# Performance work log

Hardware: AMD Instinct MI355X
Metric: run time of the kernel (lower is better)

## Reference

```python
import jax, jax.numpy as jnp
import numpy as np

SHAPE = 512
DEPTH = 9


def setup_inputs() -> dict:
    key = jax.random.key(0)
    # points with x,y in [0,1) so int(pt*SHAPE) lands in [0, SHAPE-1]
    data = jax.random.uniform(key, (8, 200000, 4), dtype=jnp.float32)
    return {"data": data}


def _group_one(pts, shape, depth):
    # pts: [N, F]. Faithful to the torch loop: scale x,y by `shape`, bin into
    # (x, y) cells, assign each nonzero point (in original point order) to the
    # first free depth slot of its cell, storing fractional coords.
    n, f = pts.shape
    scale = jnp.ones((f,), pts.dtype).at[0].set(shape).at[1].set(shape)
    scaled = pts * scale
    nonzero = jnp.any(pts != 0, axis=-1)  # all-zero points are skipped
    xi = scaled[:, 0].astype(jnp.int32)  # int() truncation == floor for [0,1)
    yi = scaled[:, 1].astype(jnp.int32)
    cell = xi * shape + yi  # [N]
    ncells = shape * shape
    # sentinel cell for zero points so they don't consume slots
    cell_k = jnp.where(nonzero, cell, ncells)
    # slot = number of earlier nonzero points in the same cell.
    # Stable sort by cell preserves point order within each cell; rank within
    # the sorted segment is (position - segment start).
    order = jnp.argsort(cell_k)  # stable
    sc = cell_k[order]
    ar = jnp.arange(n, dtype=jnp.int32)
    is_start = jnp.concatenate([jnp.ones((1,), bool), sc[1:] != sc[:-1]])
    seg_start = jax.lax.cummax(jnp.where(is_start, ar, 0))
    rank_sorted = ar - seg_start
    slot = jnp.zeros((n,), jnp.int32).at[order].set(rank_sorted)
    # fractional in-cell coordinates (pt[0]-x, pt[1]-y), other features kept
    frac = scaled.at[:, 0].add(-xi.astype(scaled.dtype)).at[:, 1].add(-yi.astype(scaled.dtype))
    valid = nonzero & (slot < depth)  # overflow points are dropped (warning in torch)
    dump = ncells * depth  # scratch row for invalid points
    flat_idx = jnp.where(valid, cell * depth + slot, dump)
    grid = jnp.zeros((ncells * depth + 1, f), scaled.dtype)
    grid = grid.at[flat_idx].set(jnp.where(valid[:, None], frac, jnp.zeros_like(frac)))
    return grid[:-1].reshape(shape, shape, depth * f)


def reference(data) -> jnp.ndarray:
    # data: [B, N, F] -> [B, SHAPE, SHAPE, DEPTH*F]
    return jax.vmap(lambda p: _group_one(p, SHAPE, DEPTH))(data)
```

## Files before the change

kernel.cpp:

```cpp
#include <hip/hip_runtime.h>
#include <stdint.h>

#define SHAPE    512
#define DEPTH    9
#define NCELLS   (SHAPE * SHAPE)
#define NB       8
#define RANGES   1024
#define CR       (NCELLS / RANGES)
#define CRSHIFT  8
#define CAP      512
#define CAPSHIFT 9
#define NCHUNK   64
#define SENT     0xFFFFFFFFu
#define EMIT     ((CR * DEPTH) / 256)

typedef float f32x4 __attribute__((ext_vector_type(4)));


__global__ void zero_heads(unsigned* __restrict__ h, int n) {
    int t = blockIdx.x * blockDim.x + threadIdx.x;
    if (t < n) h[t] = 0u;
}

__global__ __launch_bounds__(512) void bin_kernel(const float4* __restrict__ pts,
                                                  unsigned* __restrict__ headcnt,
                                                  unsigned* __restrict__ bktE,
                                                  int nPerB, int chSz) {
    __shared__ unsigned h[RANGES];
    int b = blockIdx.x & (NB - 1);
    int c = blockIdx.x >> 3;
    for (int r = threadIdx.x; r < RANGES; r += 512) h[r] = 0u;
    __syncthreads();

    int i0 = c * chSz;
    int i1 = i0 + chSz; if (i1 > nPerB) i1 = nPerB;
    const float4* pb = pts + (size_t)b * nPerB;

    for (int i = i0 + threadIdx.x; i < i1; i += 512) {
        float4 p = pb[i];
        if (p.x == 0.f && p.y == 0.f && p.z == 0.f && p.w == 0.f) continue;
        int xi = (int)(p.x * (float)SHAPE);
        int yi = (int)(p.y * (float)SHAPE);
        unsigned cell = (unsigned)(xi * SHAPE + yi);
        if (cell >= (unsigned)NCELLS) continue;
        atomicAdd(&h[cell >> CRSHIFT], 1u);
    }
    __syncthreads();

    for (int r = threadIdx.x; r < RANGES; r += 512) {
        unsigned n = h[r];
        unsigned bucket = (unsigned)(b * RANGES + r);
        unsigned base = n ? atomicAdd(&headcnt[bucket], n) : 0u;
        h[r] = (bucket << CAPSHIFT) + base;
    }
    __syncthreads();

    for (int i = i0 + threadIdx.x; i < i1; i += 512) {
        float4 p = pb[i];
        if (p.x == 0.f && p.y == 0.f && p.z == 0.f && p.w == 0.f) continue;
        int xi = (int)(p.x * (float)SHAPE);
        int yi = (int)(p.y * (float)SHAPE);
        unsigned cell = (unsigned)(xi * SHAPE + yi);
        if (cell >= (unsigned)NCELLS) continue;
        unsigned r = cell >> CRSHIFT;
        unsigned pos = atomicAdd(&h[r], 1u);
        unsigned bucket = (unsigned)(b * RANGES) + r;
        if (pos < ((bucket + 1u) << CAPSHIFT))
            bktE[pos] = ((unsigned)i << CRSHIFT) | (cell & (CR - 1));
    }
}

__global__ __launch_bounds__(256) void group_kernel(const unsigned* __restrict__ headcnt,
                                                    const unsigned* __restrict__ bktE,
                                                    const float4* __restrict__ pts,
                                                    float4* __restrict__ out,
                                                    int nPerB) {
    __shared__ unsigned slots[CR * DEPTH];
    int blk = blockIdx.x;
    int b = blk & (NB - 1);
    int r = blk >> 3;
    int gblk = b * RANGES + r;

    uint4* s4 = (uint4*)slots;
    for (int k = threadIdx.x; k < (CR * DEPTH) / 4; k += 256)
        s4[k] = make_uint4(SENT, SENT, SENT, SENT);
    __syncthreads();

    unsigned n = headcnt[gblk];
    if (n > CAP) n = CAP;
    size_t base = (size_t)gblk << CAPSHIFT;

    for (unsigned t = threadIdx.x; t < n; t += 256) {
        unsigned v = bktE[base + t];
        unsigned* s = &slots[(v & (CR - 1)) * DEPTH];
#pragma unroll
        for (int d = 0; d < DEPTH; ++d) {
            unsigned old = atomicMin(&s[d], v);
            if (old == SENT) break;
            v = (v > old) ? v : old;
        }
    }
    __syncthreads();

    const float4* pb = pts + (size_t)b * nPerB;
    float4* ob = out + ((size_t)b * NCELLS + ((size_t)r << CRSHIFT)) * DEPTH;

    unsigned key[EMIT];
#pragma unroll
    for (int k = 0; k < EMIT; ++k)
        key[k] = slots[threadIdx.x + k * 256];

    float4 pv[EMIT];
#pragma unroll
    for (int k = 0; k < EMIT; ++k)
        if (key[k] != SENT) pv[k] = pb[key[k] >> CRSHIFT];

#pragma unroll
    for (int k = 0; k < EMIT; ++k) {
        f32x4 rv = (f32x4){0.f, 0.f, 0.f, 0.f};
        if (key[k] != SENT) {
            float sx = pv[k].x * (float)SHAPE;
            float sy = pv[k].y * (float)SHAPE;
            rv.x = sx - truncf(sx);
            rv.y = sy - truncf(sy);
            rv.z = pv[k].z;
            rv.w = pv[k].w;
        }
        __builtin_nontemporal_store(rv, (f32x4*)&ob[threadIdx.x + k * 256]);
    }
}


__global__ void init_kernel(uint4* __restrict__ A, int nVec4) {
    int tid = blockIdx.x * blockDim.x + threadIdx.x;
    if (tid < nVec4) A[tid] = make_uint4(SENT, SENT, SENT, SENT);
}

__global__ void cascade_kernel(const float4* __restrict__ pts,
                               unsigned* A, int nTotal, int nPerB) {
    int tid = blockIdx.x * blockDim.x + threadIdx.x;
    if (tid >= nTotal) return;
    int b = tid / nPerB;
    int i = tid - b * nPerB;
    float4 p = pts[tid];
    if (p.x == 0.f && p.y == 0.f && p.z == 0.f && p.w == 0.f) return;
    int xi = (int)(p.x * (float)SHAPE), yi = (int)(p.y * (float)SHAPE);
    int cell = xi * SHAPE + yi;
    if ((unsigned)cell >= (unsigned)NCELLS) return;
    unsigned v = (unsigned)i;
    unsigned* base = A + (size_t)(b * NCELLS + cell) * (DEPTH * 4);
#pragma unroll
    for (int s = 0; s < DEPTH; ++s) {
        unsigned old = atomicMin(base + s * 4, v);
        if (old == SENT) break;
        v = (v > old) ? v : old;
    }
}

__global__ void write_kernel(const float4* __restrict__ pts,
                             const unsigned* A, float4* out, int nSlots, int nPerB) {
    int tid = blockIdx.x * blockDim.x + threadIdx.x;
    if (tid >= nSlots) return;
    unsigned idx = A[(size_t)tid * 4];
    float4 r = make_float4(0.f, 0.f, 0.f, 0.f);
    if (idx < (unsigned)nPerB) {
        int b = tid / (NCELLS * DEPTH);
        float4 p = pts[(size_t)b * nPerB + idx];
        float sx = p.x * (float)SHAPE, sy = p.y * (float)SHAPE;
        r.x = sx - truncf(sx); r.y = sy - truncf(sy);
        r.z = p.z; r.w = p.w;
    }
    out[tid] = r;
}

extern "C" void kernel_launch(void* const* d_in, const int* in_sizes, int n_in,
                              void* d_out, int out_size, void* d_ws, size_t ws_size,
                              hipStream_t stream) {
    const float4* pts = (const float4*)d_in[0];

    int total = in_sizes[0];
    int nPerB = total / (NB * 4);

    int nBuckets = NB * RANGES;
    size_t eBytes = (size_t)nBuckets * CAP * sizeof(unsigned);
    size_t hBytes = (size_t)nBuckets * sizeof(unsigned);
    size_t need = eBytes + hBytes;

    bool fast = (ws_size >= need) && (nPerB <= (1 << 18));
    if (fast) {
        unsigned* bktE    = (unsigned*)d_ws;
        unsigned* headcnt = (unsigned*)((char*)d_ws + eBytes);

        int chSz = (nPerB + NCHUNK - 1) / NCHUNK;

        zero_heads<<<(nBuckets + 255) / 256, 256, 0, stream>>>(headcnt, nBuckets);

        bin_kernel<<<NCHUNK * NB, 512, 0, stream>>>(pts, headcnt, bktE, nPerB, chSz);

        group_kernel<<<RANGES * NB, 256, 0, stream>>>(headcnt, bktE, pts,
                                                      (float4*)d_out, nPerB);
    } else {
        int nPts   = NB * nPerB;
        int nSlots = NB * NCELLS * DEPTH;
        unsigned* A = (unsigned*)d_out;
        int initVec4 = out_size / 4;
        init_kernel<<<(initVec4 + 255) / 256, 256, 0, stream>>>((uint4*)A, initVec4);
        cascade_kernel<<<(nPts + 255) / 256, 256, 0, stream>>>(pts, A, nPts, nPerB);
        write_kernel<<<(nSlots + 255) / 256, 256, 0, stream>>>(
            pts, A, (float4*)d_out, nSlots, nPerB);
    }
}
```

Baseline: 78.77 us.

## Scatter full point payloads into buckets and stage them in LDS for emit

The binning pass now writes each point's float4 payload next to its index into per-bucket workspace. The group kernel reads payloads contiguously, stages them in shared memory, and resolves the slot's point through a local bucket offset. This replaces the random gathers from the original point array in the emit phase. In exchange it writes 16 extra bytes per point in the bin pass, needs a larger workspace, and adds 8KB of LDS per block, which may lower occupancy.

```diff
diff --git a/kernel.cpp b/kernel.cpp
--- a/kernel.cpp
+++ b/kernel.cpp
@@ -24,7 +24,8 @@
 
 __global__ __launch_bounds__(512) void bin_kernel(const float4* __restrict__ pts,
                                                   unsigned* __restrict__ headcnt,
-                                                  unsigned* __restrict__ bktE,
+                                                  unsigned* __restrict__ bktI,
+                                                  float4* __restrict__ bktP,
                                                   int nPerB, int chSz) {
     __shared__ unsigned h[RANGES];
     int b = blockIdx.x & (NB - 1);
@@ -65,17 +66,19 @@
         unsigned r = cell >> CRSHIFT;
         unsigned pos = atomicAdd(&h[r], 1u);
         unsigned bucket = (unsigned)(b * RANGES) + r;
-        if (pos < ((bucket + 1u) << CAPSHIFT))
-            bktE[pos] = ((unsigned)i << CRSHIFT) | (cell & (CR - 1));
+        if (pos < ((bucket + 1u) << CAPSHIFT)) {
+            bktI[pos] = (unsigned)i;
+            bktP[pos] = p;
+        }
     }
 }
 
 __global__ __launch_bounds__(256) void group_kernel(const unsigned* __restrict__ headcnt,
-                                                    const unsigned* __restrict__ bktE,
-                                                    const float4* __restrict__ pts,
-                                                    float4* __restrict__ out,
-                                                    int nPerB) {
+                                                    const unsigned* __restrict__ bktI,
+                                                    const float4* __restrict__ bktP,
+                                                    float4* __restrict__ out) {
     __shared__ unsigned slots[CR * DEPTH];
+    __shared__ float4   staged[CAP];
     int blk = blockIdx.x;
     int b = blk & (NB - 1);
     int r = blk >> 3;
@@ -91,8 +94,14 @@
     size_t base = (size_t)gblk << CAPSHIFT;
 
     for (unsigned t = threadIdx.x; t < n; t += 256) {
-        unsigned v = bktE[base + t];
-        unsigned* s = &slots[(v & (CR - 1)) * DEPTH];
+        float4 p = bktP[base + t];
+        unsigned i = bktI[base + t];
+        staged[t] = p;
+        int xi = (int)(p.x * (float)SHAPE);
+        int yi = (int)(p.y * (float)SHAPE);
+        unsigned cl = ((unsigned)(xi * SHAPE + yi)) & (CR - 1);
+        unsigned v = (i << CAPSHIFT) | t;
+        unsigned* s = &slots[cl * DEPTH];
 #pragma unroll
         for (int d = 0; d < DEPTH; ++d) {
             unsigned old = atomicMin(&s[d], v);
@@ -102,29 +111,24 @@
     }
     __syncthreads();
 
-    const float4* pb = pts + (size_t)b * nPerB;
     float4* ob = out + ((size_t)b * NCELLS + ((size_t)r << CRSHIFT)) * DEPTH;
 
     unsigned key[EMIT];
 #pragma unroll
     for (int k = 0; k < EMIT; ++k)
         key[k] = slots[threadIdx.x + k * 256];
-
-    float4 pv[EMIT];
-#pragma unroll
-    for (int k = 0; k < EMIT; ++k)
-        if (key[k] != SENT) pv[k] = pb[key[k] >> CRSHIFT];
 
 #pragma unroll
     for (int k = 0; k < EMIT; ++k) {
         f32x4 rv = (f32x4){0.f, 0.f, 0.f, 0.f};
         if (key[k] != SENT) {
-            float sx = pv[k].x * (float)SHAPE;
-            float sy = pv[k].y * (float)SHAPE;
+            float4 p = staged[key[k] & (CAP - 1)];
+            float sx = p.x * (float)SHAPE;
+            float sy = p.y * (float)SHAPE;
             rv.x = sx - truncf(sx);
             rv.y = sy - truncf(sy);
-            rv.z = pv[k].z;
-            rv.w = pv[k].w;
+            rv.z = p.z;
+            rv.w = p.w;
         }
         __builtin_nontemporal_store(rv, (f32x4*)&ob[threadIdx.x + k * 256]);
     }
@@ -182,23 +186,26 @@
     int nPerB = total / (NB * 4);
 
     int nBuckets = NB * RANGES;
-    size_t eBytes = (size_t)nBuckets * CAP * sizeof(unsigned);
+    size_t pBytes = (size_t)nBuckets * CAP * sizeof(float4);
+    size_t iBytes = (size_t)nBuckets * CAP * sizeof(unsigned);
     size_t hBytes = (size_t)nBuckets * sizeof(unsigned);
-    size_t need = eBytes + hBytes;
+    size_t need = pBytes + iBytes + hBytes;
 
     bool fast = (ws_size >= need) && (nPerB <= (1 << 18));
     if (fast) {
-        unsigned* bktE    = (unsigned*)d_ws;
-        unsigned* headcnt = (unsigned*)((char*)d_ws + eBytes);
+        float4*   bktP    = (float4*)d_ws;
+        unsigned* bktI    = (unsigned*)((char*)d_ws + pBytes);
+        unsigned* headcnt = (unsigned*)((char*)d_ws + pBytes + iBytes);
 
         int chSz = (nPerB + NCHUNK - 1) / NCHUNK;
 
         zero_heads<<<(nBuckets + 255) / 256, 256, 0, stream>>>(headcnt, nBuckets);
 
-        bin_kernel<<<NCHUNK * NB, 512, 0, stream>>>(pts, headcnt, bktE, nPerB, chSz);
-
-        group_kernel<<<RANGES * NB, 256, 0, stream>>>(headcnt, bktE, pts,
-                                                      (float4*)d_out, nPerB);
+        bin_kernel<<<NCHUNK * NB, 512, 0, stream>>>(pts, headcnt, bktI, bktP,
+                                                    nPerB, chSz);
+
+        group_kernel<<<RANGES * NB, 256, 0, stream>>>(headcnt, bktI, bktP,
+                                                      (float4*)d_out);
     } else {
         int nPts   = NB * nPerB;
         int nSlots = NB * NCELLS * DEPTH;
```

New measurement: 96.02 us. 21.9% more time.
